# Kernel optimization log

Hardware: AMD Instinct MI355X
Metric: run time of the kernel (lower is better)

The kernel has to match this reference:

```python
import jax, jax.numpy as jnp
import numpy as np

N_EMBD = 1024
HEAD_SIZE = 64


def setup_inputs() -> dict:
    key = jax.random.key(0)
    k1, k2, k3, k4 = jax.random.split(key, 4)
    x = jax.random.normal(k1, (8, 2048, N_EMBD), dtype=jnp.float32)
    # torch Linear(n_embd, head_size, bias=False): y = x @ W.T with W [out,in].
    # Store as [in, out] so y = x @ W. Scale init like torch default (~1/sqrt(in)).
    s = 1.0 / np.sqrt(N_EMBD)
    Wk = jax.random.uniform(k2, (N_EMBD, HEAD_SIZE), jnp.float32, -s, s)
    Wq = jax.random.uniform(k3, (N_EMBD, HEAD_SIZE), jnp.float32, -s, s)
    Wv = jax.random.uniform(k4, (N_EMBD, HEAD_SIZE), jnp.float32, -s, s)
    return {"x": x, "Wk": Wk, "Wq": Wq, "Wv": Wv}


def reference(x, Wk, Wq, Wv):
    # x: [B,T,C]
    B, T, C = x.shape
    k = x @ Wk  # [B,T,H]
    q = x @ Wq  # [B,T,H]
    v = x @ Wv  # [B,T,H]
    scale = HEAD_SIZE ** -0.5
    wei = jnp.einsum('bth,bsh->bts', q, k) * scale  # [B,T,T]
    causal = jnp.tril(jnp.ones((T, T), dtype=bool))  # [T,T]
    wei = jnp.where(causal[None, :, :], wei, -jnp.inf)
    wei = jax.nn.softmax(wei, axis=-1)
    # dropout(p=0.2) is identity in eval mode (deterministic baseline)
    out = jnp.einsum('bts,bsh->bth', wei, v)  # [B,T,H]
    return out
```

## Files before the change

### kernel.cpp

```cpp
#include <hip/hip_runtime.h>
#include <hip/hip_bf16.h>

#define B_DIM 8
#define T_DIM 2048
#define C_DIM 1024
#define H_DIM 64
#define BT (B_DIM * T_DIM)

typedef __attribute__((ext_vector_type(8))) short bf16x8;
typedef __attribute__((ext_vector_type(4))) float f32x4;

__device__ __forceinline__ ushort f2bf(float f) {
    __hip_bfloat16 h = __float2bfloat16(f);
    return *reinterpret_cast<ushort*>(&h);
}
__device__ __forceinline__ unsigned int packbf(float a, float b) {
    return (unsigned int)f2bf(a) | ((unsigned int)f2bf(b) << 16);
}

__global__ __launch_bounds__(256) void wt_convert_kernel(
    const float* __restrict__ Wk, const float* __restrict__ Wq,
    const float* __restrict__ Wv, ushort* __restrict__ wt)
{
    __shared__ float tile[64][65];
    const int mat = blockIdx.x >> 4;
    const int k0 = (blockIdx.x & 15) << 6;
    const float* src = (mat == 0) ? Wk : (mat == 1) ? Wq : Wv;
    const float scale = (mat == 1) ? 0.125f * 1.4426950408889634f : 1.0f;
    #pragma unroll
    for (int i = 0; i < 16; ++i) {
        const int idx = i * 256 + threadIdx.x;
        const int r = idx >> 6, c = idx & 63;
        tile[r][c] = src[(size_t)(k0 + r) * H_DIM + c];
    }
    __syncthreads();
    const int c = threadIdx.x >> 2, r0 = (threadIdx.x & 3) << 4;
    unsigned int u[8];
    #pragma unroll
    for (int j = 0; j < 8; ++j)
        u[j] = packbf(tile[r0 + 2 * j][c] * scale, tile[r0 + 2 * j + 1][c] * scale);
    ushort* dst = wt + (size_t)(mat * 64 + c) * C_DIM + k0 + r0;
    *(uint4*)(dst)     = (uint4){u[0], u[1], u[2], u[3]};
    *(uint4*)(dst + 8) = (uint4){u[4], u[5], u[6], u[7]};
}

__global__ __launch_bounds__(256) void qkv_gemm_kernel(
    const float* __restrict__ x, const ushort* __restrict__ wt,
    ushort* __restrict__ kb, ushort* __restrict__ qb, ushort* __restrict__ vt)
{
    __shared__ ushort Xf[2][4 * 64 * 8];
    const int tid = threadIdx.x;
    const int wave = tid >> 6, lane = tid & 63;
    const int col = lane & 15, quad = lane >> 4;
    const int r0 = blockIdx.x * 32;

    f32x4 acc[2][3];
    #pragma unroll
    for (int m = 0; m < 2; ++m)
        #pragma unroll
        for (int i = 0; i < 3; ++i) acc[m][i] = (f32x4){0.f, 0.f, 0.f, 0.f};

    const int xrow = (wave >> 1) * 16 + col;
    const int xcc  = (wave & 1) * 4 + quad;
    const float* xsrc = x + (size_t)(r0 + xrow) * C_DIM + xcc * 8;

    const ushort* wsrc[3][2];
    #pragma unroll
    for (int j = 0; j < 3; ++j)
        #pragma unroll
        for (int ks = 0; ks < 2; ++ks)
            wsrc[j][ks] = wt + (size_t)((wave * 3 + j) * 16 + col) * C_DIM
                             + ks * 32 + quad * 8;

    {
        const float4 f0 = *(const float4*)(xsrc);
        const float4 f1 = *(const float4*)(xsrc + 4);
        uint4 u;
        u.x = packbf(f0.x, f0.y); u.y = packbf(f0.z, f0.w);
        u.z = packbf(f1.x, f1.y); u.w = packbf(f1.z, f1.w);
        *(uint4*)&Xf[0][(wave * 64 + lane) * 8] = u;
    }
    bf16x8 wcur[3][2];
    #pragma unroll
    for (int j = 0; j < 3; ++j)
        #pragma unroll
        for (int ks = 0; ks < 2; ++ks)
            wcur[j][ks] = *(const bf16x8*)(wsrc[j][ks]);
    __syncthreads();

    for (int i = 0; i < 16; ++i) {
        const int b = i & 1;
        bf16x8 wnxt[3][2];
        float4 nf0, nf1;
        if (i < 15) {
            const int k1 = (i + 1) * 64;
            #pragma unroll
            for (int j = 0; j < 3; ++j)
                #pragma unroll
                for (int ks = 0; ks < 2; ++ks)
                    wnxt[j][ks] = *(const bf16x8*)(wsrc[j][ks] + k1);
            nf0 = *(const float4*)(xsrc + k1);
            nf1 = *(const float4*)(xsrc + k1 + 4);
        }
        #pragma unroll
        for (int ks = 0; ks < 2; ++ks) {
            const bf16x8 a0 = *(const bf16x8*)&Xf[b][((    ks) * 64 + lane) * 8];
            const bf16x8 a1 = *(const bf16x8*)&Xf[b][((2 + ks) * 64 + lane) * 8];
            #pragma unroll
            for (int j = 0; j < 3; ++j) {
                acc[0][j] = __builtin_amdgcn_mfma_f32_16x16x32_bf16(a0, wcur[j][ks], acc[0][j], 0, 0, 0);
                acc[1][j] = __builtin_amdgcn_mfma_f32_16x16x32_bf16(a1, wcur[j][ks], acc[1][j], 0, 0, 0);
            }
        }
        if (i < 15) {
            #pragma unroll
            for (int j = 0; j < 3; ++j)
                #pragma unroll
                for (int ks = 0; ks < 2; ++ks)
                    wcur[j][ks] = wnxt[j][ks];
            uint4 u;
            u.x = packbf(nf0.x, nf0.y); u.y = packbf(nf0.z, nf0.w);
            u.z = packbf(nf1.x, nf1.y); u.w = packbf(nf1.z, nf1.w);
            *(uint4*)&Xf[b ^ 1][(wave * 64 + lane) * 8] = u;
        }
        __syncthreads();
    }

    #pragma unroll
    for (int i = 0; i < 3; ++i) {
        const int nt = wave * 3 + i;
        #pragma unroll
        for (int mf = 0; mf < 2; ++mf) {
            const int rbase = r0 + mf * 16 + quad * 4;
            if (nt < 4) {
                const int n = nt * 16 + col;
                #pragma unroll
                for (int r = 0; r < 4; ++r)
                    kb[(size_t)(rbase + r) * H_DIM + n] = f2bf(acc[mf][i][r]);
            } else if (nt < 8) {
                const int n = nt * 16 + col - 64;
                #pragma unroll
                for (int r = 0; r < 4; ++r)
                    qb[(size_t)(rbase + r) * H_DIM + n] = f2bf(acc[mf][i][r]);
            } else {
                const int h = nt * 16 + col - 128;
                const int vbatch = rbase >> 11, vrow = rbase & (T_DIM - 1);
                ushort u4[4] = {f2bf(acc[mf][i][0]), f2bf(acc[mf][i][1]),
                                f2bf(acc[mf][i][2]), f2bf(acc[mf][i][3])};
                unsigned long long uu; __builtin_memcpy(&uu, u4, 8);
                *(unsigned long long*)(vt + ((size_t)vbatch * H_DIM + h) * T_DIM + vrow) = uu;
            }
        }
    }
}

__global__ __launch_bounds__(256) void attn_kernel(
    const ushort* __restrict__ kb, const ushort* __restrict__ qb,
    const ushort* __restrict__ vt, float* __restrict__ out)
{
    __shared__ unsigned int Ps[4][16 * 34];
    __shared__ float Om[4][64][17];
    __shared__ float Mm[4][16], Lm[4][16];

    const int tid = threadIdx.x;
    const int wave = tid >> 6, lane = tid & 63;
    const int col = lane & 15, quad = lane >> 4;
    const int batch = blockIdx.x & 7;
    const int qtile = 127 - (blockIdx.x >> 3);
    const int q0 = qtile * 16;

    const ushort* kbase = kb + (size_t)batch * T_DIM * H_DIM;
    const ushort* vbase = vt + (size_t)batch * H_DIM * T_DIM;

    const size_t qoff = (size_t)(batch * T_DIM + q0 + col) * H_DIM + quad * 8;
    const bf16x8 bq0 = *(const bf16x8*)(qb + qoff);
    const bf16x8 bq1 = *(const bf16x8*)(qb + qoff + 32);

    float m_ = -INFINITY, l_ = 0.f;
    f32x4 o_[4];
    #pragma unroll
    for (int i = 0; i < 4; ++i) o_[i] = (f32x4){0.f, 0.f, 0.f, 0.f};

    const int ntiles = (q0 + 16 + 63) >> 6;
    unsigned int* psw = &Ps[wave][0];

    for (int t = wave; t < ntiles; t += 4) {
        const int kb0 = t * 64;
        f32x4 s[4];
        #pragma unroll
        for (int mt = 0; mt < 4; ++mt) s[mt] = (f32x4){0.f, 0.f, 0.f, 0.f};
        __builtin_amdgcn_s_setprio(1);
        #pragma unroll
        for (int ks = 0; ks < 2; ++ks) {
            const bf16x8 bq = ks ? bq1 : bq0;
            #pragma unroll
            for (int mt = 0; mt < 4; ++mt) {
                const bf16x8 ak = *(const bf16x8*)
                    (kbase + (size_t)(kb0 + mt * 16 + col) * H_DIM + ks * 32 + quad * 8);
                s[mt] = __builtin_amdgcn_mfma_f32_16x16x32_bf16(ak, bq, s[mt], 0, 0, 0);
            }
        }
        __builtin_amdgcn_s_setprio(0);
        if (kb0 + 63 > q0) {
            const int kq = kb0 + quad * 4 - q0 - col;
            #pragma unroll
            for (int mt = 0; mt < 4; ++mt)
                #pragma unroll
                for (int reg = 0; reg < 4; ++reg)
                    if (kq + mt * 16 + reg > 0) s[mt][reg] = -INFINITY;
        }
        float mr;
        {
            const float a = fmaxf(s[0][0], s[0][1]), b = fmaxf(s[0][2], s[0][3]);
            const float c = fmaxf(s[1][0], s[1][1]), d = fmaxf(s[1][2], s[1][3]);
            const float e = fmaxf(s[2][0], s[2][1]), f = fmaxf(s[2][2], s[2][3]);
            const float g = fmaxf(s[3][0], s[3][1]), h = fmaxf(s[3][2], s[3][3]);
            mr = fmaxf(fmaxf(fmaxf(a, b), fmaxf(c, d)),
                       fmaxf(fmaxf(e, f), fmaxf(g, h)));
        }
        mr = fmaxf(mr, __shfl_xor(mr, 16));
        mr = fmaxf(mr, __shfl_xor(mr, 32));
        if (__any(mr > m_ + 8.f)) {
            const float mn = fmaxf(m_, mr);
            const float corr = __builtin_amdgcn_exp2f(m_ - mn);
            l_ *= corr;
            #pragma unroll
            for (int ht = 0; ht < 4; ++ht) o_[ht] *= corr;
            m_ = mn;
        }
        float psum[4];
        #pragma unroll
        for (int mt = 0; mt < 4; ++mt) {
            #pragma unroll
            for (int reg = 0; reg < 4; ++reg)
                s[mt][reg] = __builtin_amdgcn_exp2f(s[mt][reg] - m_);
            psum[mt] = (s[mt][0] + s[mt][1]) + (s[mt][2] + s[mt][3]);
        }
        float sum = (psum[0] + psum[1]) + (psum[2] + psum[3]);
        sum += __shfl_xor(sum, 16);
        sum += __shfl_xor(sum, 32);
        l_ += sum;
        #pragma unroll
        for (int mt = 0; mt < 4; ++mt) {
            uint2 w2;
            w2.x = packbf(s[mt][0], s[mt][1]);
            w2.y = packbf(s[mt][2], s[mt][3]);
            *(uint2*)&psw[col * 34 + mt * 8 + quad * 2] = w2;
        }
        __builtin_amdgcn_s_setprio(1);
        #pragma unroll
        for (int ks2 = 0; ks2 < 2; ++ks2) {
            const uint2 ra = *(const uint2*)&psw[col * 34 + ks2 * 16 + quad * 4];
            const uint2 rb = *(const uint2*)&psw[col * 34 + ks2 * 16 + quad * 4 + 2];
            unsigned int ub[4] = {ra.x, ra.y, rb.x, rb.y};
            bf16x8 bp; __builtin_memcpy(&bp, ub, 16);
            #pragma unroll
            for (int ht = 0; ht < 4; ++ht) {
                const bf16x8 av = *(const bf16x8*)
                    (vbase + (size_t)(ht * 16 + col) * T_DIM + kb0 + ks2 * 32 + quad * 8);
                o_[ht] = __builtin_amdgcn_mfma_f32_16x16x32_bf16(av, bp, o_[ht], 0, 0, 0);
            }
        }
        __builtin_amdgcn_s_setprio(0);
    }

    #pragma unroll
    for (int ht = 0; ht < 4; ++ht)
        #pragma unroll
        for (int reg = 0; reg < 4; ++reg)
            Om[wave][ht * 16 + quad * 4 + reg][col] = o_[ht][reg];
    if (lane < 16) { Mm[wave][lane] = m_; Lm[wave][lane] = l_; }
    __syncthreads();
    {
        const int q = tid >> 4, hb = tid & 15;
        const float M = fmaxf(fmaxf(Mm[0][q], Mm[1][q]), fmaxf(Mm[2][q], Mm[3][q]));
        const float a0 = __builtin_amdgcn_exp2f(Mm[0][q] - M);
        const float a1 = __builtin_amdgcn_exp2f(Mm[1][q] - M);
        const float a2 = __builtin_amdgcn_exp2f(Mm[2][q] - M);
        const float a3 = __builtin_amdgcn_exp2f(Mm[3][q] - M);
        const float L = Lm[0][q] * a0 + Lm[1][q] * a1 + Lm[2][q] * a2 + Lm[3][q] * a3;
        const float rL = 1.0f / L;
        float* orow = out + (size_t)(batch * T_DIM + q0 + q) * H_DIM;
        #pragma unroll
        for (int i = 0; i < 4; ++i) {
            const int h = hb + 16 * i;
            orow[h] = (Om[0][h][q] * a0 + Om[1][h][q] * a1 +
                       Om[2][h][q] * a2 + Om[3][h][q] * a3) * rL;
        }
    }
}

extern "C" void kernel_launch(void* const* d_in, const int* in_sizes, int n_in,
                              void* d_out, int out_size, void* d_ws, size_t ws_size,
                              hipStream_t stream)
{
    const float* x  = (const float*)d_in[0];
    const float* Wk = (const float*)d_in[1];
    const float* Wq = (const float*)d_in[2];
    const float* Wv = (const float*)d_in[3];

    ushort* kbuf = (ushort*)d_ws;
    ushort* qbuf = kbuf + (size_t)BT * H_DIM;
    ushort* vtb  = qbuf + (size_t)BT * H_DIM;
    ushort* wt   = vtb  + (size_t)BT * H_DIM;

    wt_convert_kernel<<<48, 256, 0, stream>>>(Wk, Wq, Wv, wt);
    qkv_gemm_kernel<<<BT / 32, 256, 0, stream>>>(x, wt, kbuf, qbuf, vtb);
    attn_kernel<<<B_DIM * 128, 256, 0, stream>>>(kbuf, qbuf, vtb, (float*)d_out);
}
```

Before: 159.2 us.

## Drop LDS staging in QKV GEMM and hoist K/V loads in attention loop

In the QKV projection kernel, the shared-memory double buffer and per-iteration barriers are removed. Each wave now loads its x fragments straight from global memory into registers, converts them to bf16 there, and ping-pongs two register buffers through a fully unrolled k-loop. In the attention kernel, all K and V fragments for a tile are loaded at the top of the iteration, so their latency overlaps the QK MFMAs and the softmax. The trade is that every wave now reads x redundantly instead of sharing it through LDS, register pressure rises, and occupancy may drop.

```diff
diff --git a/kernel.cpp b/kernel.cpp
--- a/kernel.cpp
+++ b/kernel.cpp
@@ -16,6 +16,11 @@
 }
 __device__ __forceinline__ unsigned int packbf(float a, float b) {
     return (unsigned int)f2bf(a) | ((unsigned int)f2bf(b) << 16);
+}
+__device__ __forceinline__ bf16x8 pack8(float4 a, float4 b) {
+    unsigned int u[4] = {packbf(a.x, a.y), packbf(a.z, a.w),
+                         packbf(b.x, b.y), packbf(b.z, b.w)};
+    bf16x8 r; __builtin_memcpy(&r, u, 16); return r;
 }
 
 __global__ __launch_bounds__(256) void wt_convert_kernel(
@@ -44,11 +49,40 @@
     *(uint4*)(dst + 8) = (uint4){u[4], u[5], u[6], u[7]};
 }
 
+#define QKV_LOAD(XB, WB, I) do {                                            \
+    const int k1_ = (I) * 64;                                               \
+    _Pragma("unroll")                                                       \
+    for (int mf_ = 0; mf_ < 2; ++mf_)                                       \
+        _Pragma("unroll")                                                   \
+        for (int ks_ = 0; ks_ < 2; ++ks_) {                                 \
+            XB[(mf_ * 2 + ks_) * 2]     = *(const float4*)(xa[mf_][ks_] + k1_);     \
+            XB[(mf_ * 2 + ks_) * 2 + 1] = *(const float4*)(xa[mf_][ks_] + k1_ + 4); \
+        }                                                                   \
+    _Pragma("unroll")                                                       \
+    for (int j_ = 0; j_ < 3; ++j_)                                          \
+        _Pragma("unroll")                                                   \
+        for (int ks_ = 0; ks_ < 2; ++ks_)                                   \
+            WB[j_ * 2 + ks_] = *(const bf16x8*)(wsrc[j_][ks_] + k1_);       \
+} while (0)
+
+#define QKV_COMPUTE(XB, WB) do {                                            \
+    _Pragma("unroll")                                                       \
+    for (int mf_ = 0; mf_ < 2; ++mf_)                                       \
+        _Pragma("unroll")                                                   \
+        for (int ks_ = 0; ks_ < 2; ++ks_) {                                 \
+            const bf16x8 af_ = pack8(XB[(mf_ * 2 + ks_) * 2],               \
+                                     XB[(mf_ * 2 + ks_) * 2 + 1]);          \
+            _Pragma("unroll")                                               \
+            for (int j_ = 0; j_ < 3; ++j_)                                  \
+                acc[mf_][j_] = __builtin_amdgcn_mfma_f32_16x16x32_bf16(     \
+                    af_, WB[j_ * 2 + ks_], acc[mf_][j_], 0, 0, 0);          \
+        }                                                                   \
+} while (0)
+
 __global__ __launch_bounds__(256) void qkv_gemm_kernel(
     const float* __restrict__ x, const ushort* __restrict__ wt,
     ushort* __restrict__ kb, ushort* __restrict__ qb, ushort* __restrict__ vt)
 {
-    __shared__ ushort Xf[2][4 * 64 * 8];
     const int tid = threadIdx.x;
     const int wave = tid >> 6, lane = tid & 63;
     const int col = lane & 15, quad = lane >> 4;
@@ -60,9 +94,12 @@
         #pragma unroll
         for (int i = 0; i < 3; ++i) acc[m][i] = (f32x4){0.f, 0.f, 0.f, 0.f};
 
-    const int xrow = (wave >> 1) * 16 + col;
-    const int xcc  = (wave & 1) * 4 + quad;
-    const float* xsrc = x + (size_t)(r0 + xrow) * C_DIM + xcc * 8;
+    const float* xa[2][2];
+    #pragma unroll
+    for (int mf = 0; mf < 2; ++mf)
+        #pragma unroll
+        for (int ks = 0; ks < 2; ++ks)
+            xa[mf][ks] = x + (size_t)(r0 + mf * 16 + col) * C_DIM + ks * 32 + quad * 8;
 
     const ushort* wsrc[3][2];
     #pragma unroll
@@ -72,58 +109,16 @@
             wsrc[j][ks] = wt + (size_t)((wave * 3 + j) * 16 + col) * C_DIM
                              + ks * 32 + quad * 8;
 
-    {
-        const float4 f0 = *(const float4*)(xsrc);
-        const float4 f1 = *(const float4*)(xsrc + 4);
-        uint4 u;
-        u.x = packbf(f0.x, f0.y); u.y = packbf(f0.z, f0.w);
-        u.z = packbf(f1.x, f1.y); u.w = packbf(f1.z, f1.w);
-        *(uint4*)&Xf[0][(wave * 64 + lane) * 8] = u;
-    }
-    bf16x8 wcur[3][2];
-    #pragma unroll
-    for (int j = 0; j < 3; ++j)
-        #pragma unroll
-        for (int ks = 0; ks < 2; ++ks)
-            wcur[j][ks] = *(const bf16x8*)(wsrc[j][ks]);
-    __syncthreads();
-
-    for (int i = 0; i < 16; ++i) {
-        const int b = i & 1;
-        bf16x8 wnxt[3][2];
-        float4 nf0, nf1;
-        if (i < 15) {
-            const int k1 = (i + 1) * 64;
-            #pragma unroll
-            for (int j = 0; j < 3; ++j)
-                #pragma unroll
-                for (int ks = 0; ks < 2; ++ks)
-                    wnxt[j][ks] = *(const bf16x8*)(wsrc[j][ks] + k1);
-            nf0 = *(const float4*)(xsrc + k1);
-            nf1 = *(const float4*)(xsrc + k1 + 4);
-        }
-        #pragma unroll
-        for (int ks = 0; ks < 2; ++ks) {
-            const bf16x8 a0 = *(const bf16x8*)&Xf[b][((    ks) * 64 + lane) * 8];
-            const bf16x8 a1 = *(const bf16x8*)&Xf[b][((2 + ks) * 64 + lane) * 8];
-            #pragma unroll
-            for (int j = 0; j < 3; ++j) {
-                acc[0][j] = __builtin_amdgcn_mfma_f32_16x16x32_bf16(a0, wcur[j][ks], acc[0][j], 0, 0, 0);
-                acc[1][j] = __builtin_amdgcn_mfma_f32_16x16x32_bf16(a1, wcur[j][ks], acc[1][j], 0, 0, 0);
-            }
-        }
-        if (i < 15) {
-            #pragma unroll
-            for (int j = 0; j < 3; ++j)
-                #pragma unroll
-                for (int ks = 0; ks < 2; ++ks)
-                    wcur[j][ks] = wnxt[j][ks];
-            uint4 u;
-            u.x = packbf(nf0.x, nf0.y); u.y = packbf(nf0.z, nf0.w);
-            u.z = packbf(nf1.x, nf1.y); u.w = packbf(nf1.z, nf1.w);
-            *(uint4*)&Xf[b ^ 1][(wave * 64 + lane) * 8] = u;
-        }
-        __syncthreads();
+    float4 xA[8], xB[8];
+    bf16x8 wA[6], wB[6];
+
+    QKV_LOAD(xA, wA, 0);
+    #pragma unroll
+    for (int ii = 0; ii < 8; ++ii) {
+        if (2 * ii + 1 < 16) QKV_LOAD(xB, wB, 2 * ii + 1);
+        QKV_COMPUTE(xA, wA);
+        if (2 * ii + 2 < 16) QKV_LOAD(xA, wA, 2 * ii + 2);
+        QKV_COMPUTE(xB, wB);
     }
 
     #pragma unroll
@@ -186,6 +181,20 @@
 
     for (int t = wave; t < ntiles; t += 4) {
         const int kb0 = t * 64;
+        bf16x8 ak[2][4];
+        #pragma unroll
+        for (int ks = 0; ks < 2; ++ks)
+            #pragma unroll
+            for (int mt = 0; mt < 4; ++mt)
+                ak[ks][mt] = *(const bf16x8*)
+                    (kbase + (size_t)(kb0 + mt * 16 + col) * H_DIM + ks * 32 + quad * 8);
+        bf16x8 av[2][4];
+        #pragma unroll
+        for (int ks2 = 0; ks2 < 2; ++ks2)
+            #pragma unroll
+            for (int ht = 0; ht < 4; ++ht)
+                av[ks2][ht] = *(const bf16x8*)
+                    (vbase + (size_t)(ht * 16 + col) * T_DIM + kb0 + ks2 * 32 + quad * 8);
         f32x4 s[4];
         #pragma unroll
         for (int mt = 0; mt < 4; ++mt) s[mt] = (f32x4){0.f, 0.f, 0.f, 0.f};
@@ -194,11 +203,8 @@
         for (int ks = 0; ks < 2; ++ks) {
             const bf16x8 bq = ks ? bq1 : bq0;
             #pragma unroll
-            for (int mt = 0; mt < 4; ++mt) {
-                const bf16x8 ak = *(const bf16x8*)
-                    (kbase + (size_t)(kb0 + mt * 16 + col) * H_DIM + ks * 32 + quad * 8);
-                s[mt] = __builtin_amdgcn_mfma_f32_16x16x32_bf16(ak, bq, s[mt], 0, 0, 0);
-            }
+            for (int mt = 0; mt < 4; ++mt)
+                s[mt] = __builtin_amdgcn_mfma_f32_16x16x32_bf16(ak[ks][mt], bq, s[mt], 0, 0, 0);
         }
         __builtin_amdgcn_s_setprio(0);
         if (kb0 + 63 > q0) {
@@ -255,11 +261,8 @@
             unsigned int ub[4] = {ra.x, ra.y, rb.x, rb.y};
             bf16x8 bp; __builtin_memcpy(&bp, ub, 16);
             #pragma unroll
-            for (int ht = 0; ht < 4; ++ht) {
-                const bf16x8 av = *(const bf16x8*)
-                    (vbase + (size_t)(ht * 16 + col) * T_DIM + kb0 + ks2 * 32 + quad * 8);
-                o_[ht] = __builtin_amdgcn_mfma_f32_16x16x32_bf16(av, bp, o_[ht], 0, 0, 0);
-            }
+            for (int ht = 0; ht < 4; ++ht)
+                o_[ht] = __builtin_amdgcn_mfma_f32_16x16x32_bf16(av[ks2][ht], bp, o_[ht], 0, 0, 0);
         }
         __builtin_amdgcn_s_setprio(0);
     }
```

Measured after the change: 178.3 us. 12.0% more time.

## Share K/V tiles in LDS across four query waves and pre-tile weights

Applied to the files above, without the earlier changes.

The attention kernel now gives each block 64 query rows, one 16-row slice per wave. All four waves share a K/V tile that is double-buffered and XOR-swizzled in LDS and prefetched one tile ahead. This replaces the old scheme where the waves split the key range of a single 16-row query tile, so the cross-wave softmax merge through shared memory goes away. Separately, the weight-convert kernel writes weights in a fragment-tiled order so GEMM weight loads become contiguous per lane. The trade-offs are fewer blocks (256 instead of 1024), which lowers parallelism and worsens causal load balance, plus a block-wide barrier on every key tile.

```diff
diff --git a/kernel.cpp b/kernel.cpp
--- a/kernel.cpp
+++ b/kernel.cpp
@@ -24,7 +24,8 @@
 {
     __shared__ float tile[64][65];
     const int mat = blockIdx.x >> 4;
-    const int k0 = (blockIdx.x & 15) << 6;
+    const int s   = blockIdx.x & 15;
+    const int k0  = s << 6;
     const float* src = (mat == 0) ? Wk : (mat == 1) ? Wq : Wv;
     const float scale = (mat == 1) ? 0.125f * 1.4426950408889634f : 1.0f;
     #pragma unroll
@@ -34,14 +35,20 @@
         tile[r][c] = src[(size_t)(k0 + r) * H_DIM + c];
     }
     __syncthreads();
-    const int c = threadIdx.x >> 2, r0 = (threadIdx.x & 3) << 4;
-    unsigned int u[8];
-    #pragma unroll
-    for (int j = 0; j < 8; ++j)
-        u[j] = packbf(tile[r0 + 2 * j][c] * scale, tile[r0 + 2 * j + 1][c] * scale);
-    ushort* dst = wt + (size_t)(mat * 64 + c) * C_DIM + k0 + r0;
-    *(uint4*)(dst)     = (uint4){u[0], u[1], u[2], u[3]};
-    *(uint4*)(dst + 8) = (uint4){u[4], u[5], u[6], u[7]};
+    const int ntl = threadIdx.x >> 6, lane = threadIdx.x & 63;
+    const int col = lane & 15, quad = lane >> 4;
+    const int nt = mat * 4 + ntl;
+    const int w = nt / 3, j = nt % 3;
+    #pragma unroll
+    for (int ks = 0; ks < 2; ++ks) {
+        unsigned int u[4];
+        #pragma unroll
+        for (int p = 0; p < 4; ++p)
+            u[p] = packbf(tile[ks * 32 + quad * 8 + 2 * p][ntl * 16 + col] * scale,
+                          tile[ks * 32 + quad * 8 + 2 * p + 1][ntl * 16 + col] * scale);
+        ushort* dst = wt + (size_t)((((s * 4 + w) * 3 + j) * 2 + ks) * 512) + lane * 8;
+        *(uint4*)dst = (uint4){u[0], u[1], u[2], u[3]};
+    }
 }
 
 __global__ __launch_bounds__(256) void qkv_gemm_kernel(
@@ -69,8 +76,7 @@
     for (int j = 0; j < 3; ++j)
         #pragma unroll
         for (int ks = 0; ks < 2; ++ks)
-            wsrc[j][ks] = wt + (size_t)((wave * 3 + j) * 16 + col) * C_DIM
-                             + ks * 32 + quad * 8;
+            wsrc[j][ks] = wt + (size_t)(((wave * 3 + j) * 2 + ks) * 512) + lane * 8;
 
     {
         const float4 f0 = *(const float4*)(xsrc);
@@ -94,11 +100,12 @@
         float4 nf0, nf1;
         if (i < 15) {
             const int k1 = (i + 1) * 64;
+            const size_t wo = (size_t)(i + 1) * 12288;
             #pragma unroll
             for (int j = 0; j < 3; ++j)
                 #pragma unroll
                 for (int ks = 0; ks < 2; ++ks)
-                    wnxt[j][ks] = *(const bf16x8*)(wsrc[j][ks] + k1);
+                    wnxt[j][ks] = *(const bf16x8*)(wsrc[j][ks] + wo);
             nf0 = *(const float4*)(xsrc + k1);
             nf1 = *(const float4*)(xsrc + k1 + 4);
         }
@@ -158,21 +165,28 @@
     const ushort* __restrict__ kb, const ushort* __restrict__ qb,
     const ushort* __restrict__ vt, float* __restrict__ out)
 {
+    __shared__ ushort Kt[2][64][64];
+    __shared__ ushort Vt[2][64][64];
     __shared__ unsigned int Ps[4][16 * 34];
-    __shared__ float Om[4][64][17];
-    __shared__ float Mm[4][16], Lm[4][16];
 
     const int tid = threadIdx.x;
     const int wave = tid >> 6, lane = tid & 63;
     const int col = lane & 15, quad = lane >> 4;
     const int batch = blockIdx.x & 7;
-    const int qtile = 127 - (blockIdx.x >> 3);
-    const int q0 = qtile * 16;
+    const int qt = 31 - (blockIdx.x >> 3);
+    const int q0 = qt * 64;
+    const int ntiles = qt + 1;
+    const int qmy = q0 + wave * 16;
 
     const ushort* kbase = kb + (size_t)batch * T_DIM * H_DIM;
     const ushort* vbase = vt + (size_t)batch * H_DIM * T_DIM;
 
-    const size_t qoff = (size_t)(batch * T_DIM + q0 + col) * H_DIM + quad * 8;
+    const int srow0 = tid >> 3, srow1 = 32 + (tid >> 3);
+    const int scb = tid & 7;
+    const int sdst0 = (scb ^ (srow0 & 7)) * 8;
+    const int sdst1 = (scb ^ (srow1 & 7)) * 8;
+
+    const size_t qoff = (size_t)(batch * T_DIM + qmy + col) * H_DIM + quad * 8;
     const bf16x8 bq0 = *(const bf16x8*)(qb + qoff);
     const bf16x8 bq1 = *(const bf16x8*)(qb + qoff + 32);
 
@@ -181,11 +195,32 @@
     #pragma unroll
     for (int i = 0; i < 4; ++i) o_[i] = (f32x4){0.f, 0.f, 0.f, 0.f};
 
-    const int ntiles = (q0 + 16 + 63) >> 6;
     unsigned int* psw = &Ps[wave][0];
 
-    for (int t = wave; t < ntiles; t += 4) {
+    {
+        const uint4 a0 = *(const uint4*)(kbase + (size_t)srow0 * H_DIM + scb * 8);
+        const uint4 a1 = *(const uint4*)(kbase + (size_t)srow1 * H_DIM + scb * 8);
+        const uint4 b0 = *(const uint4*)(vbase + (size_t)srow0 * T_DIM + scb * 8);
+        const uint4 b1 = *(const uint4*)(vbase + (size_t)srow1 * T_DIM + scb * 8);
+        *(uint4*)&Kt[0][srow0][sdst0] = a0;
+        *(uint4*)&Kt[0][srow1][sdst1] = a1;
+        *(uint4*)&Vt[0][srow0][sdst0] = b0;
+        *(uint4*)&Vt[0][srow1][sdst1] = b1;
+    }
+    __syncthreads();
+
+    for (int t = 0; t < ntiles; ++t) {
+        const int b = t & 1;
         const int kb0 = t * 64;
+        const bool pf = (t + 1 < ntiles);
+        uint4 nk0, nk1, nv0, nv1;
+        if (pf) {
+            const int kb1 = kb0 + 64;
+            nk0 = *(const uint4*)(kbase + (size_t)(kb1 + srow0) * H_DIM + scb * 8);
+            nk1 = *(const uint4*)(kbase + (size_t)(kb1 + srow1) * H_DIM + scb * 8);
+            nv0 = *(const uint4*)(vbase + (size_t)srow0 * T_DIM + kb1 + scb * 8);
+            nv1 = *(const uint4*)(vbase + (size_t)srow1 * T_DIM + kb1 + scb * 8);
+        }
         f32x4 s[4];
         #pragma unroll
         for (int mt = 0; mt < 4; ++mt) s[mt] = (f32x4){0.f, 0.f, 0.f, 0.f};
@@ -195,14 +230,14 @@
             const bf16x8 bq = ks ? bq1 : bq0;
             #pragma unroll
             for (int mt = 0; mt < 4; ++mt) {
-                const bf16x8 ak = *(const bf16x8*)
-                    (kbase + (size_t)(kb0 + mt * 16 + col) * H_DIM + ks * 32 + quad * 8);
+                const int row = mt * 16 + col;
+                const bf16x8 ak = *(const bf16x8*)&Kt[b][row][((ks * 4 + quad) ^ (row & 7)) * 8];
                 s[mt] = __builtin_amdgcn_mfma_f32_16x16x32_bf16(ak, bq, s[mt], 0, 0, 0);
             }
         }
         __builtin_amdgcn_s_setprio(0);
-        if (kb0 + 63 > q0) {
-            const int kq = kb0 + quad * 4 - q0 - col;
+        if (kb0 + 63 > qmy) {
+            const int kq = kb0 + quad * 4 - qmy - col;
             #pragma unroll
             for (int mt = 0; mt < 4; ++mt)
                 #pragma unroll
@@ -211,11 +246,11 @@
         }
         float mr;
         {
-            const float a = fmaxf(s[0][0], s[0][1]), b = fmaxf(s[0][2], s[0][3]);
+            const float a = fmaxf(s[0][0], s[0][1]), bb = fmaxf(s[0][2], s[0][3]);
             const float c = fmaxf(s[1][0], s[1][1]), d = fmaxf(s[1][2], s[1][3]);
             const float e = fmaxf(s[2][0], s[2][1]), f = fmaxf(s[2][2], s[2][3]);
             const float g = fmaxf(s[3][0], s[3][1]), h = fmaxf(s[3][2], s[3][3]);
-            mr = fmaxf(fmaxf(fmaxf(a, b), fmaxf(c, d)),
+            mr = fmaxf(fmaxf(fmaxf(a, bb), fmaxf(c, d)),
                        fmaxf(fmaxf(e, f), fmaxf(g, h)));
         }
         mr = fmaxf(mr, __shfl_xor(mr, 16));
@@ -256,38 +291,28 @@
             bf16x8 bp; __builtin_memcpy(&bp, ub, 16);
             #pragma unroll
             for (int ht = 0; ht < 4; ++ht) {
-                const bf16x8 av = *(const bf16x8*)
-                    (vbase + (size_t)(ht * 16 + col) * T_DIM + kb0 + ks2 * 32 + quad * 8);
+                const int row = ht * 16 + col;
+                const bf16x8 av = *(const bf16x8*)&Vt[b][row][((ks2 * 4 + quad) ^ (row & 7)) * 8];
                 o_[ht] = __builtin_amdgcn_mfma_f32_16x16x32_bf16(av, bp, o_[ht], 0, 0, 0);
             }
         }
         __builtin_amdgcn_s_setprio(0);
-    }
-
+        if (pf) {
+            *(uint4*)&Kt[b ^ 1][srow0][sdst0] = nk0;
+            *(uint4*)&Kt[b ^ 1][srow1][sdst1] = nk1;
+            *(uint4*)&Vt[b ^ 1][srow0][sdst0] = nv0;
+            *(uint4*)&Vt[b ^ 1][srow1][sdst1] = nv1;
+        }
+        __syncthreads();
+    }
+
+    const float rL = 1.0f / l_;
+    float* orow = out + (size_t)(batch * T_DIM + qmy + col) * H_DIM;
     #pragma unroll
     for (int ht = 0; ht < 4; ++ht)
         #pragma unroll
         for (int reg = 0; reg < 4; ++reg)
-            Om[wave][ht * 16 + quad * 4 + reg][col] = o_[ht][reg];
-    if (lane < 16) { Mm[wave][lane] = m_; Lm[wave][lane] = l_; }
-    __syncthreads();
-    {
-        const int q = tid >> 4, hb = tid & 15;
-        const float M = fmaxf(fmaxf(Mm[0][q], Mm[1][q]), fmaxf(Mm[2][q], Mm[3][q]));
-        const float a0 = __builtin_amdgcn_exp2f(Mm[0][q] - M);
-        const float a1 = __builtin_amdgcn_exp2f(Mm[1][q] - M);
-        const float a2 = __builtin_amdgcn_exp2f(Mm[2][q] - M);
-        const float a3 = __builtin_amdgcn_exp2f(Mm[3][q] - M);
-        const float L = Lm[0][q] * a0 + Lm[1][q] * a1 + Lm[2][q] * a2 + Lm[3][q] * a3;
-        const float rL = 1.0f / L;
-        float* orow = out + (size_t)(batch * T_DIM + q0 + q) * H_DIM;
-        #pragma unroll
-        for (int i = 0; i < 4; ++i) {
-            const int h = hb + 16 * i;
-            orow[h] = (Om[0][h][q] * a0 + Om[1][h][q] * a1 +
-                       Om[2][h][q] * a2 + Om[3][h][q] * a3) * rL;
-        }
-    }
+            orow[ht * 16 + quad * 4 + reg] = o_[ht][reg] * rL;
 }
 
 extern "C" void kernel_launch(void* const* d_in, const int* in_sizes, int n_in,
@@ -306,5 +331,5 @@
 
     wt_convert_kernel<<<48, 256, 0, stream>>>(Wk, Wq, Wv, wt);
     qkv_gemm_kernel<<<BT / 32, 256, 0, stream>>>(x, wt, kbuf, qbuf, vtb);
-    attn_kernel<<<B_DIM * 128, 256, 0, stream>>>(kbuf, qbuf, vtb, (float*)d_out);
-}
+    attn_kernel<<<B_DIM * 32, 256, 0, stream>>>(kbuf, qbuf, vtb, (float*)d_out);
+}
```

New measurement: 158.6 us. Within noise of the previous version (-0.4%).
